# Performance work log

Hardware: AMD Instinct MI355X
Metric: run time of the kernel (lower is better)

Reference implementation:

```python
import jax, jax.numpy as jnp
import numpy as np

NUM_HEAD = 16
DIM_HEAD = 64
SCALE = DIM_HEAD ** -0.5


def setup_inputs() -> dict:
    key = jax.random.key(0)
    k1, k2, k3 = jax.random.split(key, 3)
    B, N, D = 4, 2048, 1024
    x = jax.random.normal(k1, (B, N, D), dtype=jnp.float32)
    w_qkv = jax.random.normal(k2, (D, 3 * NUM_HEAD * DIM_HEAD), dtype=jnp.float32) * (D ** -0.5)
    w_out = jax.random.normal(k3, (NUM_HEAD * DIM_HEAD, D), dtype=jnp.float32) * ((NUM_HEAD * DIM_HEAD) ** -0.5)
    return {"x": x, "w_qkv": w_qkv, "w_out": w_out}


def reference(x, w_qkv, w_out):
    B, N, D = x.shape
    qkv = x @ w_qkv  # [B, N, 3*H*Dh]
    q, k, v = jnp.split(qkv, 3, axis=-1)
    def heads(t):
        return t.reshape(B, N, NUM_HEAD, DIM_HEAD).transpose(0, 2, 1, 3)  # b h n d
    q, k, v = heads(q), heads(k), heads(v)
    scores = jnp.einsum('bhnd,bhmd->bhnm', q, k) * SCALE
    attn = jax.nn.softmax(scores, axis=-1)
    out = jnp.einsum('bhnm,bhmd->bhnd', attn, v)
    out = out.transpose(0, 2, 1, 3).reshape(B, N, NUM_HEAD * DIM_HEAD)
    return out @ w_out
```

## Files before the change

### kernel.cpp

```cpp
#include <hip/hip_runtime.h>
#include <hip/hip_bf16.h>
#include <stdint.h>


typedef __attribute__((ext_vector_type(8))) __bf16 bf16x8;
typedef __attribute__((ext_vector_type(4))) __bf16 bf16x4;
typedef __attribute__((ext_vector_type(4))) float f32x4;
typedef __attribute__((ext_vector_type(16))) float f32x16;
typedef __attribute__((ext_vector_type(4))) unsigned int u32x4;

#define EXPC 0.18033688011112042f
#define THRR 64.0f

static __device__ __forceinline__ void gload_lds16(const void* g, void* s) {
  __builtin_amdgcn_global_load_lds(
      (__attribute__((address_space(1))) unsigned int*)g,
      (__attribute__((address_space(3))) unsigned int*)s, 16, 0, 0);
}

static __device__ __forceinline__ unsigned pk2(float lo, float hi) {
  unsigned short a = __builtin_bit_cast(unsigned short, (__bf16)lo);
  unsigned short b = __builtin_bit_cast(unsigned short, (__bf16)hi);
  return (unsigned)a | ((unsigned)b << 16);
}

__global__ void k_cvt(const float* __restrict__ src, __bf16* __restrict__ dst, int n4) {
  int i = blockIdx.x * blockDim.x + threadIdx.x;
  if (i >= n4) return;
  float4 v = reinterpret_cast<const float4*>(src)[i];
  bf16x4 o = { (__bf16)v.x, (__bf16)v.y, (__bf16)v.z, (__bf16)v.w };
  *reinterpret_cast<bf16x4*>(dst + (size_t)i * 4) = o;
}

__global__ void k_tcvt(const float* __restrict__ src, __bf16* __restrict__ dst, int W, int Hs) {
  __shared__ float tile[32][33];
  int tx = threadIdx.x, ty = threadIdx.y;
  int x = blockIdx.x * 32 + tx;
  int y0 = blockIdx.y * 32;
  for (int j = ty; j < 32; j += 8) tile[j][tx] = src[(size_t)(y0 + j) * W + x];
  __syncthreads();
  int xo = y0 + tx;
  int yo = blockIdx.x * 32;
  for (int j = ty; j < 32; j += 8) dst[(size_t)(yo + j) * Hs + xo] = (__bf16)tile[tx][j];
}

static __device__ __forceinline__ void gemm_core(
    const __bf16* __restrict__ A, const __bf16* __restrict__ BT, int K,
    int m0, int n0, f32x4 acc[4][4], __bf16* As, __bf16* Bs) {
  const int tid = threadIdx.x;
  const int lane = tid & 63, w = tid >> 6;
  const int fr = lane & 15, fq = lane >> 4;
  const int srow = lane >> 2, scol = (lane & 3) * 8;
  const int wr = (w >> 1) * 64, wc = (w & 1) * 64;
#pragma unroll
  for (int mi = 0; mi < 4; ++mi)
#pragma unroll
    for (int nj = 0; nj < 4; ++nj) acc[mi][nj] = (f32x4){0.f, 0.f, 0.f, 0.f};

  for (int ko = 0; ko < K; ko += 32) {
#pragma unroll
    for (int i = 0; i < 2; ++i) {
      int rb = w * 32 + i * 16;
      gload_lds16(A + (size_t)(m0 + rb + srow) * K + ko + scol, As + rb * 32);
      gload_lds16(BT + (size_t)(n0 + rb + srow) * K + ko + scol, Bs + rb * 32);
    }
    __syncthreads();
    bf16x8 af[4], bfv[4];
#pragma unroll
    for (int mi = 0; mi < 4; ++mi)
      af[mi] = *(const bf16x8*)(As + (wr + mi * 16 + fr) * 32 + fq * 8);
#pragma unroll
    for (int nj = 0; nj < 4; ++nj)
      bfv[nj] = *(const bf16x8*)(Bs + (wc + nj * 16 + fr) * 32 + fq * 8);
#pragma unroll
    for (int mi = 0; mi < 4; ++mi)
#pragma unroll
      for (int nj = 0; nj < 4; ++nj)
        acc[mi][nj] = __builtin_amdgcn_mfma_f32_16x16x32_bf16(af[mi], bfv[nj], acc[mi][nj], 0, 0, 0);
    __syncthreads();
  }
}

__global__ __launch_bounds__(256) void k_gemm_qkv(
    const __bf16* __restrict__ A, const __bf16* __restrict__ BT,
    __bf16* __restrict__ qb, __bf16* __restrict__ kb, __bf16* __restrict__ vb) {
  __shared__ __align__(16) __bf16 As[128 * 32];
  __shared__ __align__(16) __bf16 Bs[128 * 32];
  f32x4 acc[4][4];
  int m0 = blockIdx.x * 128, n0 = blockIdx.y * 128;
  gemm_core(A, BT, 1024, m0, n0, acc, As, Bs);
  const int lane = threadIdx.x & 63, w = threadIdx.x >> 6;
  const int fr = lane & 15, fq = lane >> 4;
  const int wr = (w >> 1) * 64, wc = (w & 1) * 64;
  const int which = n0 >> 10;
#pragma unroll
  for (int mi = 0; mi < 4; ++mi) {
#pragma unroll
    for (int nj = 0; nj < 4; ++nj) {
      int row = m0 + wr + mi * 16 + fq * 4;
      int col = n0 + wc + nj * 16 + fr;
      int rem = col & 1023, h = rem >> 6, d = rem & 63;
      int bb = row >> 11, n = row & 2047;
      int bh = bb * 16 + h;
      if (which == 2) {
        bf16x4 pk = { (__bf16)acc[mi][nj][0], (__bf16)acc[mi][nj][1],
                      (__bf16)acc[mi][nj][2], (__bf16)acc[mi][nj][3] };
        *reinterpret_cast<bf16x4*>(vb + ((size_t)bh * 64 + d) * 2048 + n) = pk;
      } else {
        __bf16* dst = (which == 0) ? qb : kb;
#pragma unroll
        for (int j = 0; j < 4; ++j)
          dst[((size_t)bh * 2048 + (n + j)) * 64 + d] = (__bf16)acc[mi][nj][j];
      }
    }
  }
}

__global__ __launch_bounds__(256) void k_gemm_out(
    const __bf16* __restrict__ A, const __bf16* __restrict__ BT, float* __restrict__ C) {
  __shared__ __align__(16) __bf16 As[128 * 32];
  __shared__ __align__(16) __bf16 Bs[128 * 32];
  f32x4 acc[4][4];
  int m0 = blockIdx.x * 128, n0 = blockIdx.y * 128;
  gemm_core(A, BT, 1024, m0, n0, acc, As, Bs);
  const int lane = threadIdx.x & 63, w = threadIdx.x >> 6;
  const int fr = lane & 15, fq = lane >> 4;
  const int wr = (w >> 1) * 64, wc = (w & 1) * 64;
#pragma unroll
  for (int mi = 0; mi < 4; ++mi)
#pragma unroll
    for (int nj = 0; nj < 4; ++nj)
#pragma unroll
      for (int j = 0; j < 4; ++j)
        C[(size_t)(m0 + wr + mi * 16 + fq * 4 + j) * 1024 + n0 + wc + nj * 16 + fr] =
            acc[mi][nj][j];
}

__global__ __launch_bounds__(256, 3) void k_attn(
    const __bf16* __restrict__ qb, const __bf16* __restrict__ kb,
    const __bf16* __restrict__ vb, __bf16* __restrict__ ao) {
  __shared__ __align__(16) __bf16 Ks[2][64 * 64];
  __shared__ __align__(16) __bf16 Vs[2][64 * 64];
  const int tid = threadIdx.x, lane = tid & 63, wid = tid >> 6;
  const int r31 = lane & 31, hi = lane >> 5;
  const int lsw = (lane & 7) ^ ((lane >> 3) & 3);
  const int bh = blockIdx.x & 63, qblk = blockIdx.x >> 6;
  const __bf16* kbase = kb + (size_t)bh * 2048 * 64;
  const __bf16* vbase = vb + (size_t)bh * 64 * 2048;

  const int nbase = qblk * 128 + wid * 32;
  const __bf16* qptr = qb + ((size_t)bh * 2048 + nbase + r31) * 64;
  bf16x8 qf[4];
#pragma unroll
  for (int dd = 0; dd < 4; ++dd)
    qf[dd] = *(const bf16x8*)(qptr + dd * 16 + hi * 8);

  f32x16 o0, o1;
#pragma unroll
  for (int r = 0; r < 16; ++r) { o0[r] = 0.f; o1[r] = 0.f; }
  float m = -1e30f, lsum = 0.f;

  auto stage = [&](int buf, int j0) {
#pragma unroll
    for (int p2 = 0; p2 < 2; ++p2) {
      int row = p2 * 32 + (tid >> 3);
      int sc = (tid & 7) ^ (row & 7) ^ ((row >> 3) & 3);
      int dst = p2 * 2048 + wid * 512;
      gload_lds16(kbase + (size_t)(j0 + row) * 64 + sc * 8, &Ks[buf][dst]);
      gload_lds16(vbase + (size_t)row * 2048 + j0 + sc * 8, &Vs[buf][dst]);
    }
  };

  stage(0, 0);
  __syncthreads();

  for (int kt = 0; kt < 32; ++kt) {
    const int cur = kt & 1;
    if (kt < 31) stage(cur ^ 1, (kt + 1) * 64);

    f32x16 sa0, sa1;
#pragma unroll
    for (int r = 0; r < 16; ++r) { sa0[r] = 0.f; sa1[r] = 0.f; }
    __builtin_amdgcn_s_setprio(1);
#pragma unroll
    for (int dd = 0; dd < 4; ++dd) {
      bf16x8 k0 = *(const bf16x8*)(&Ks[cur][r31 * 64 + (((dd * 2 + hi) ^ lsw) << 3)]);
      bf16x8 k1 = *(const bf16x8*)(&Ks[cur][(32 + r31) * 64 + (((dd * 2 + hi) ^ lsw) << 3)]);
      sa0 = __builtin_amdgcn_mfma_f32_32x32x16_bf16(k0, qf[dd], sa0, 0, 0, 0);
      sa1 = __builtin_amdgcn_mfma_f32_32x32x16_bf16(k1, qf[dd], sa1, 0, 0, 0);
    }
    __builtin_amdgcn_s_setprio(0);

    float mx[8];
#pragma unroll
    for (int r = 0; r < 8; ++r)
      mx[r] = fmaxf(fmaxf(fmaxf(sa0[2 * r], sa0[2 * r + 1]), sa1[2 * r]), sa1[2 * r + 1]);
#pragma unroll
    for (int s = 4; s > 0; s >>= 1)
#pragma unroll
      for (int r = 0; r < s; ++r) mx[r] = fmaxf(mx[r], mx[r + s]);
    float pmax = fmaxf(mx[0], __shfl_xor(mx[0], 32, 64));

    if (!__all(pmax - m <= THRR)) {
      float mn = fmaxf(m, pmax);
      float corr = __builtin_amdgcn_exp2f((m - mn) * EXPC);
      m = mn;
      lsum *= corr;
#pragma unroll
      for (int r = 0; r < 16; ++r) {
        int qrow = (r & 3) + 8 * (r >> 2) + 4 * hi;
        float cr = __shfl(corr, qrow, 64);
        o0[r] *= cr; o1[r] *= cr;
      }
    }

    const float mneg = -m * EXPC;
    float rs0 = 0.f, rs1 = 0.f, rs2 = 0.f, rs3 = 0.f;
    unsigned pw0[8], pw1[8];
#pragma unroll
    for (int r = 0; r < 8; ++r) {
      float e0 = __builtin_amdgcn_exp2f(fmaf(sa0[2 * r], EXPC, mneg));
      float e1 = __builtin_amdgcn_exp2f(fmaf(sa0[2 * r + 1], EXPC, mneg));
      float e2 = __builtin_amdgcn_exp2f(fmaf(sa1[2 * r], EXPC, mneg));
      float e3 = __builtin_amdgcn_exp2f(fmaf(sa1[2 * r + 1], EXPC, mneg));
      rs0 += e0; rs1 += e1; rs2 += e2; rs3 += e3;
      pw0[r] = pk2(e0, e1);
      pw1[r] = pk2(e2, e3);
    }
    lsum += (rs0 + rs1) + (rs2 + rs3);

    unsigned f[4][4];
#pragma unroll
    for (int ks = 0; ks < 2; ++ks) {
      unsigned a0 = pw0[ks * 4 + 0], a1 = pw0[ks * 4 + 1];
      unsigned b0 = pw0[ks * 4 + 2], b1 = pw0[ks * 4 + 3];
      asm("v_permlane32_swap_b32 %0, %1" : "+v"(a0), "+v"(b0));
      asm("v_permlane32_swap_b32 %0, %1" : "+v"(a1), "+v"(b1));
      f[ks][0] = a0; f[ks][1] = a1; f[ks][2] = b0; f[ks][3] = b1;
      unsigned c0 = pw1[ks * 4 + 0], c1 = pw1[ks * 4 + 1];
      unsigned d0 = pw1[ks * 4 + 2], d1 = pw1[ks * 4 + 3];
      asm("v_permlane32_swap_b32 %0, %1" : "+v"(c0), "+v"(d0));
      asm("v_permlane32_swap_b32 %0, %1" : "+v"(c1), "+v"(d1));
      f[2 + ks][0] = c0; f[2 + ks][1] = c1; f[2 + ks][2] = d0; f[2 + ks][3] = d1;
    }

    __builtin_amdgcn_s_setprio(1);
#pragma unroll
    for (int kk = 0; kk < 4; ++kk) {
      u32x4 fw = {f[kk][0], f[kk][1], f[kk][2], f[kk][3]};
      bf16x8 pa = __builtin_bit_cast(bf16x8, fw);
      bf16x8 v0 = *(const bf16x8*)(&Vs[cur][r31 * 64 + (((kk * 2 + hi) ^ lsw) << 3)]);
      bf16x8 v1 = *(const bf16x8*)(&Vs[cur][(32 + r31) * 64 + (((kk * 2 + hi) ^ lsw) << 3)]);
      o0 = __builtin_amdgcn_mfma_f32_32x32x16_bf16(pa, v0, o0, 0, 0, 0);
      o1 = __builtin_amdgcn_mfma_f32_32x32x16_bf16(pa, v1, o1, 0, 0, 0);
    }
    __builtin_amdgcn_s_setprio(0);

    __syncthreads();
  }

  lsum += __shfl_xor(lsum, 32, 64);
  float inv = 1.0f / lsum;
  const int b = bh >> 4, h = bh & 15;
  __bf16* abase = ao + ((size_t)b * 2048 + nbase) * 1024 + h * 64 + r31;
#pragma unroll
  for (int r = 0; r < 16; ++r) {
    int qrow = (r & 3) + 8 * (r >> 2) + 4 * hi;
    float ir = __shfl(inv, qrow, 64);
    abase[(size_t)qrow * 1024] = (__bf16)(o0[r] * ir);
    abase[(size_t)qrow * 1024 + 32] = (__bf16)(o1[r] * ir);
  }
}

extern "C" void kernel_launch(void* const* d_in, const int* in_sizes, int n_in,
                              void* d_out, int out_size, void* d_ws, size_t ws_size,
                              hipStream_t stream) {
  (void)in_sizes; (void)n_in; (void)out_size; (void)ws_size;
  const float* x = (const float*)d_in[0];
  const float* w_qkv = (const float*)d_in[1];
  const float* w_out = (const float*)d_in[2];
  float* out = (float*)d_out;

  char* p = (char*)d_ws;
  __bf16* xb    = (__bf16*)p; p += (size_t)8192 * 1024 * 2;
  __bf16* wqkvT = (__bf16*)p; p += (size_t)3072 * 1024 * 2;
  __bf16* woutT = (__bf16*)p; p += (size_t)1024 * 1024 * 2;
  __bf16* qb    = (__bf16*)p; p += (size_t)64 * 2048 * 64 * 2;
  __bf16* kb    = (__bf16*)p; p += (size_t)64 * 2048 * 64 * 2;
  __bf16* vb    = (__bf16*)p; p += (size_t)64 * 64 * 2048 * 2;
  __bf16* ao    = (__bf16*)p; p += (size_t)8192 * 1024 * 2;

  k_cvt<<<8192, 256, 0, stream>>>(x, xb, 2097152);
  k_tcvt<<<dim3(96, 32), dim3(32, 8), 0, stream>>>(w_qkv, wqkvT, 3072, 1024);
  k_tcvt<<<dim3(32, 32), dim3(32, 8), 0, stream>>>(w_out, woutT, 1024, 1024);
  k_gemm_qkv<<<dim3(64, 24), 256, 0, stream>>>(xb, wqkvT, qb, kb, vb);
  k_attn<<<dim3(1024), dim3(256), 0, stream>>>(qb, kb, vb, ao);
  k_gemm_out<<<dim3(64, 8), 256, 0, stream>>>(ao, woutT, out);
}
```

Before: 215.2 us.

## Use 256x256 tiles with triple-buffered LDS pipeline for projection GEMMs

Replaces the 128x128 single-stage GEMM core with a 256x256 tile computed by 8 waves, staged through a three-buffer LDS ring so global loads for future k-steps overlap MFMA work. Adds an XOR swizzle on LDS rows to reduce bank conflicts and raises wave priority around the MFMA block. The larger tile cuts global traffic per FLOP but shrinks the grid, notably to 128 blocks for the output projection, which can leave compute units idle and increases register pressure.

```diff
diff --git a/kernel.cpp b/kernel.cpp
--- a/kernel.cpp
+++ b/kernel.cpp
@@ -44,61 +44,90 @@
   for (int j = ty; j < 32; j += 8) dst[(size_t)(yo + j) * Hs + xo] = (__bf16)tile[tx][j];
 }
 
-static __device__ __forceinline__ void gemm_core(
-    const __bf16* __restrict__ A, const __bf16* __restrict__ BT, int K,
-    int m0, int n0, f32x4 acc[4][4], __bf16* As, __bf16* Bs) {
+static __device__ __forceinline__ void gemm256_core(
+    const __bf16* __restrict__ A, const __bf16* __restrict__ BT,
+    int m0, int n0, f32x4 acc[8][4], __bf16* S) {
   const int tid = threadIdx.x;
-  const int lane = tid & 63, w = tid >> 6;
+  const int lane = tid & 63, wid = tid >> 6;
   const int fr = lane & 15, fq = lane >> 4;
-  const int srow = lane >> 2, scol = (lane & 3) * 8;
-  const int wr = (w >> 1) * 64, wc = (w & 1) * 64;
-#pragma unroll
-  for (int mi = 0; mi < 4; ++mi)
+  const int wm = wid >> 2, wn = wid & 3;
+  const int rsw = (fr >> 1) & 3;
+  const int srow = tid >> 2;
+  const int scs = (tid & 3) ^ ((tid >> 3) & 3);
+  const int sdst = wid * 512;
+
+#pragma unroll
+  for (int mi = 0; mi < 8; ++mi)
 #pragma unroll
     for (int nj = 0; nj < 4; ++nj) acc[mi][nj] = (f32x4){0.f, 0.f, 0.f, 0.f};
 
-  for (int ko = 0; ko < K; ko += 32) {
+  auto stage = [&](int buf, int kt) {
+    __bf16* Sa = S + buf * 16384;
+    __bf16* Sb = Sa + 8192;
 #pragma unroll
     for (int i = 0; i < 2; ++i) {
-      int rb = w * 32 + i * 16;
-      gload_lds16(A + (size_t)(m0 + rb + srow) * K + ko + scol, As + rb * 32);
-      gload_lds16(BT + (size_t)(n0 + rb + srow) * K + ko + scol, Bs + rb * 32);
-    }
-    __syncthreads();
-    bf16x8 af[4], bfv[4];
-#pragma unroll
-    for (int mi = 0; mi < 4; ++mi)
-      af[mi] = *(const bf16x8*)(As + (wr + mi * 16 + fr) * 32 + fq * 8);
+      gload_lds16(A  + (size_t)(m0 + i * 128 + srow) * 1024 + kt * 32 + scs * 8,
+                  Sa + i * 4096 + sdst);
+      gload_lds16(BT + (size_t)(n0 + i * 128 + srow) * 1024 + kt * 32 + scs * 8,
+                  Sb + i * 4096 + sdst);
+    }
+  };
+
+  stage(0, 0);
+  stage(1, 1);
+  asm volatile("s_waitcnt vmcnt(4)" ::: "memory");
+  __builtin_amdgcn_s_barrier();
+  __builtin_amdgcn_sched_barrier(0);
+
+  int cur = 0;
+  for (int kt = 0; kt < 32; ++kt) {
+    if (kt + 2 < 32) {
+      int nb = cur + 2; if (nb >= 3) nb -= 3;
+      stage(nb, kt + 2);
+    }
+    const __bf16* Sa = S + cur * 16384;
+    const __bf16* Sb = Sa + 8192;
+    bf16x8 bfv[4], af[8];
 #pragma unroll
     for (int nj = 0; nj < 4; ++nj)
-      bfv[nj] = *(const bf16x8*)(Bs + (wc + nj * 16 + fr) * 32 + fq * 8);
-#pragma unroll
-    for (int mi = 0; mi < 4; ++mi)
+      bfv[nj] = *(const bf16x8*)(Sb + (wn * 64 + nj * 16 + fr) * 32 + ((fq ^ rsw) << 3));
+#pragma unroll
+    for (int mi = 0; mi < 8; ++mi)
+      af[mi] = *(const bf16x8*)(Sa + (wm * 128 + mi * 16 + fr) * 32 + ((fq ^ rsw) << 3));
+    __builtin_amdgcn_s_setprio(1);
+#pragma unroll
+    for (int mi = 0; mi < 8; ++mi)
 #pragma unroll
       for (int nj = 0; nj < 4; ++nj)
         acc[mi][nj] = __builtin_amdgcn_mfma_f32_16x16x32_bf16(af[mi], bfv[nj], acc[mi][nj], 0, 0, 0);
-    __syncthreads();
+    __builtin_amdgcn_s_setprio(0);
+    if (kt < 31) {
+      if (kt < 30) asm volatile("s_waitcnt vmcnt(4)" ::: "memory");
+      else         asm volatile("s_waitcnt vmcnt(0)" ::: "memory");
+      __builtin_amdgcn_s_barrier();
+      __builtin_amdgcn_sched_barrier(0);
+    }
+    cur = cur + 1 == 3 ? 0 : cur + 1;
   }
 }
 
-__global__ __launch_bounds__(256) void k_gemm_qkv(
+__global__ __launch_bounds__(512, 1) void k_gemm_qkv(
     const __bf16* __restrict__ A, const __bf16* __restrict__ BT,
     __bf16* __restrict__ qb, __bf16* __restrict__ kb, __bf16* __restrict__ vb) {
-  __shared__ __align__(16) __bf16 As[128 * 32];
-  __shared__ __align__(16) __bf16 Bs[128 * 32];
-  f32x4 acc[4][4];
-  int m0 = blockIdx.x * 128, n0 = blockIdx.y * 128;
-  gemm_core(A, BT, 1024, m0, n0, acc, As, Bs);
-  const int lane = threadIdx.x & 63, w = threadIdx.x >> 6;
+  __shared__ __align__(16) __bf16 S[3 * 2 * 8192];
+  f32x4 acc[8][4];
+  int m0 = blockIdx.x * 256, n0 = blockIdx.y * 256;
+  gemm256_core(A, BT, m0, n0, acc, S);
+  const int lane = threadIdx.x & 63, wid = threadIdx.x >> 6;
   const int fr = lane & 15, fq = lane >> 4;
-  const int wr = (w >> 1) * 64, wc = (w & 1) * 64;
+  const int wm = wid >> 2, wn = wid & 3;
   const int which = n0 >> 10;
 #pragma unroll
-  for (int mi = 0; mi < 4; ++mi) {
+  for (int mi = 0; mi < 8; ++mi) {
 #pragma unroll
     for (int nj = 0; nj < 4; ++nj) {
-      int row = m0 + wr + mi * 16 + fq * 4;
-      int col = n0 + wc + nj * 16 + fr;
+      int row = m0 + wm * 128 + mi * 16 + fq * 4;
+      int col = n0 + wn * 64 + nj * 16 + fr;
       int rem = col & 1023, h = rem >> 6, d = rem & 63;
       int bb = row >> 11, n = row & 2047;
       int bh = bb * 16 + h;
@@ -116,23 +145,22 @@
   }
 }
 
-__global__ __launch_bounds__(256) void k_gemm_out(
+__global__ __launch_bounds__(512, 1) void k_gemm_out(
     const __bf16* __restrict__ A, const __bf16* __restrict__ BT, float* __restrict__ C) {
-  __shared__ __align__(16) __bf16 As[128 * 32];
-  __shared__ __align__(16) __bf16 Bs[128 * 32];
-  f32x4 acc[4][4];
-  int m0 = blockIdx.x * 128, n0 = blockIdx.y * 128;
-  gemm_core(A, BT, 1024, m0, n0, acc, As, Bs);
-  const int lane = threadIdx.x & 63, w = threadIdx.x >> 6;
+  __shared__ __align__(16) __bf16 S[3 * 2 * 8192];
+  f32x4 acc[8][4];
+  int m0 = blockIdx.x * 256, n0 = blockIdx.y * 256;
+  gemm256_core(A, BT, m0, n0, acc, S);
+  const int lane = threadIdx.x & 63, wid = threadIdx.x >> 6;
   const int fr = lane & 15, fq = lane >> 4;
-  const int wr = (w >> 1) * 64, wc = (w & 1) * 64;
-#pragma unroll
-  for (int mi = 0; mi < 4; ++mi)
+  const int wm = wid >> 2, wn = wid & 3;
+#pragma unroll
+  for (int mi = 0; mi < 8; ++mi)
 #pragma unroll
     for (int nj = 0; nj < 4; ++nj)
 #pragma unroll
       for (int j = 0; j < 4; ++j)
-        C[(size_t)(m0 + wr + mi * 16 + fq * 4 + j) * 1024 + n0 + wc + nj * 16 + fr] =
+        C[(size_t)(m0 + wm * 128 + mi * 16 + fq * 4 + j) * 1024 + n0 + wn * 64 + nj * 16 + fr] =
             acc[mi][nj][j];
 }
 
@@ -293,7 +321,7 @@
   k_cvt<<<8192, 256, 0, stream>>>(x, xb, 2097152);
   k_tcvt<<<dim3(96, 32), dim3(32, 8), 0, stream>>>(w_qkv, wqkvT, 3072, 1024);
   k_tcvt<<<dim3(32, 32), dim3(32, 8), 0, stream>>>(w_out, woutT, 1024, 1024);
-  k_gemm_qkv<<<dim3(64, 24), 256, 0, stream>>>(xb, wqkvT, qb, kb, vb);
+  k_gemm_qkv<<<dim3(32, 12), 512, 0, stream>>>(xb, wqkvT, qb, kb, vb);
   k_attn<<<dim3(1024), dim3(256), 0, stream>>>(qb, kb, vb, ao);
-  k_gemm_out<<<dim3(64, 8), 256, 0, stream>>>(ao, woutT, out);
-}
+  k_gemm_out<<<dim3(32, 4), 512, 0, stream>>>(ao, woutT, out);
+}
```

Result: no change. 218.7 us (+1.6%).
